# Kernel optimization log

Hardware: AMD Instinct MI355X
Metric: run time of the kernel (lower is better)

The kernel has to match this reference:

```python
import jax, jax.numpy as jnp
import numpy as np

B, S, D = 1, 2048, 2048
H = 16
HD = D // H           # 128
FFN_H = 5632          # int(2*4*D/3) rounded up to multiple of 256
EPS = 1e-5
ROPE_THETA = 10000.0


def rms_norm(x, w, eps=EPS):
    # x * rsqrt(mean(x^2, -1) + eps) * w
    return x * jax.lax.rsqrt(jnp.mean(x * x, axis=-1, keepdims=True) + eps) * w


def apply_rope(x, cos, sin):
    # x: [B, S, H, HD]; cos/sin: [S, HD//2]
    b, s, h, hd = x.shape
    xr = x.reshape(b, s, h, hd // 2, 2)
    x_re, x_im = xr[..., 0], xr[..., 1]
    c = cos[None, :, None, :]
    sn = sin[None, :, None, :]
    o_re = x_re * c - x_im * sn
    o_im = x_re * sn + x_im * c
    return jnp.stack([o_re, o_im], axis=-1).reshape(b, s, h, hd)


def setup_inputs() -> dict:
    key = jax.random.key(0)
    ks = jax.random.split(key, 10)
    x = jax.random.normal(ks[0], (B, S, D), dtype=jnp.float32)
    # RoPE frequencies (Llama-style)
    inv_freq = 1.0 / (ROPE_THETA ** (np.arange(0, HD, 2, dtype=np.float32) / HD))
    angles = np.outer(np.arange(S, dtype=np.float32), inv_freq)  # [S, HD//2]
    freqs_cos = jnp.asarray(np.cos(angles), dtype=jnp.float32)
    freqs_sin = jnp.asarray(np.sin(angles), dtype=jnp.float32)
    # causal mask: 1 = keep, 0 = masked
    mask = jnp.tril(jnp.ones((S, S), dtype=jnp.int32))[None, None]
    sc = 0.02
    return {
        "x": x,
        "freqs_cos": freqs_cos,
        "freqs_sin": freqs_sin,
        "mask": mask,
        "wq": jax.random.normal(ks[1], (D, D), jnp.float32) * sc,
        "wk": jax.random.normal(ks[2], (D, D), jnp.float32) * sc,
        "wv": jax.random.normal(ks[3], (D, D), jnp.float32) * sc,
        "wo": jax.random.normal(ks[4], (D, D), jnp.float32) * sc,
        "w1": jax.random.normal(ks[5], (D, FFN_H), jnp.float32) * sc,
        "w2": jax.random.normal(ks[6], (FFN_H, D), jnp.float32) * sc,
        "w3": jax.random.normal(ks[7], (D, FFN_H), jnp.float32) * sc,
        "attn_norm_w": jnp.ones((D,), jnp.float32),
        "ffn_norm_w": jnp.ones((D,), jnp.float32),
    }


def reference(x, freqs_cos, freqs_sin, mask, wq, wk, wv, wo, w1, w2, w3,
              attn_norm_w, ffn_norm_w):
    b, s, d = x.shape
    # --- attention block ---
    xn = rms_norm(x, attn_norm_w)
    q = (xn @ wq).reshape(b, s, H, HD)
    k = (xn @ wk).reshape(b, s, H, HD)
    v = (xn @ wv).reshape(b, s, H, HD)
    q = apply_rope(q, freqs_cos, freqs_sin)
    k = apply_rope(k, freqs_cos, freqs_sin)
    scores = jnp.einsum('bqhd,bkhd->bhqk', q, k) / jnp.sqrt(jnp.float32(HD))
    scores = jnp.where(mask == 0, -jnp.inf, scores)
    probs = jax.nn.softmax(scores, axis=-1)
    attn = jnp.einsum('bhqk,bkhd->bqhd', probs, v).reshape(b, s, d)
    h = x + attn @ wo
    # --- SwiGLU FFN block ---
    hn = rms_norm(h, ffn_norm_w)
    ff = (jax.nn.silu(hn @ w1) * (hn @ w3)) @ w2
    return h + ff
```

## Files before the change

kernel.cpp:

```cpp
#include <hip/hip_runtime.h>
#include <hip/hip_bf16.h>

typedef __bf16 bf16x8 __attribute__((ext_vector_type(8)));
typedef float f32x4 __attribute__((ext_vector_type(4)));
typedef unsigned short u16x8 __attribute__((ext_vector_type(8)));
typedef unsigned short u16x4 __attribute__((ext_vector_type(4)));

#define DEV static __device__ __forceinline__

DEV unsigned short f2bf(float f) {
    unsigned u = __builtin_bit_cast(unsigned, f);
    u += 0x7fffu + ((u >> 16) & 1u);
    return (unsigned short)(u >> 16);
}
DEV float bf2f(unsigned short h) {
    unsigned u = ((unsigned)h) << 16;
    return __builtin_bit_cast(float, u);
}

DEV void gl2lds16(const void* g, void* l) {
    __builtin_amdgcn_global_load_lds(
        (const __attribute__((address_space(1))) void*)g,
        (__attribute__((address_space(3))) void*)l, 16, 0, 0);
}

#define WAITV(N) asm volatile("s_waitcnt vmcnt(" #N ")" ::: "memory")
#define SBAR()   asm volatile("s_barrier" ::: "memory")

#define STAGE128D(KT, BUF)                                                    \
    _Pragma("unroll")                                                         \
    for (int sl = 0; sl < 3; ++sl) {                                          \
        const unsigned short* sbase = (sl == 0)                               \
            ? A  + (size_t)bm * K                                             \
            : BT + (size_t)(bn + (sl - 1) * 128) * K;                         \
        _Pragma("unroll")                                                     \
        for (int j = 0; j < 2; ++j) {                                         \
            const unsigned short* g = sbase + (size_t)(srow + j * 64) * K     \
                                      + koff + (KT) * 64 + lc;                \
            gl2lds16(g, &lds[BUF][sl][wave * 512 + j * 4096]);                \
        }                                                                     \
    }

#define DSREAD_K(BUF, KK, AR, BR)                                             \
    {                                                                         \
        const char* Ab = (const char*)&lds[BUF][0][0];                        \
        const char* Bb = (const char*)&lds[BUF][1 + (wn >> 1)][0];            \
        _Pragma("unroll")                                                     \
        for (int m4 = 0; m4 < 4; ++m4)                                        \
            AR[m4] = *(const bf16x8*)(Ab +                                    \
                (wm * 64 + m4 * 16 + lr) * 128 +                              \
                (((KK) * 64 + lg * 16) ^ xsw));                               \
        _Pragma("unroll")                                                     \
        for (int n2 = 0; n2 < 4; ++n2)                                        \
            BR[n2] = *(const bf16x8*)(Bb +                                    \
                ((wn & 1) * 64 + n2 * 16 + lr) * 128 +                        \
                (((KK) * 64 + lg * 16) ^ xsw));                               \
    }

#define MFMA16(AR, BR)                                                        \
    __builtin_amdgcn_s_setprio(1);                                            \
    _Pragma("unroll")                                                         \
    for (int m4 = 0; m4 < 4; ++m4)                                            \
        _Pragma("unroll")                                                     \
        for (int n2 = 0; n2 < 4; ++n2)                                        \
            acc[m4][n2] = __builtin_amdgcn_mfma_f32_16x16x32_bf16(            \
                AR[m4], BR[n2], acc[m4][n2], 0, 0, 0);                        \
    __builtin_amdgcn_s_setprio(0);

template <int EPI>
__global__ __launch_bounds__(512, 2)
void gemm128d(const unsigned short* __restrict__ A,
              const unsigned short* __restrict__ BT,
              unsigned short* __restrict__ outB,
              float* __restrict__ outP,
              int M, int N, int K,
              const float* __restrict__ cs, const float* __restrict__ sn,
              unsigned short* __restrict__ vT)
{
    __shared__ alignas(16) unsigned short lds[3][3][8192];
    const int tid  = threadIdx.x;
    const int lane = tid & 63;
    const int wave = tid >> 6;
    const int wm = wave >> 2;
    const int wn = wave & 3;
    const int lr = lane & 15;
    const int lg = lane >> 4;
    const int gy  = gridDim.y;
    const int lin = blockIdx.y * gridDim.x + blockIdx.x;
    const int cpx = (gridDim.x * gy) >> 3;
    const int swz = (lin & 7) * cpx + (lin >> 3);
    const int bm = (swz % gy) * 128;
    const int bn = (swz / gy) * 256;
    const int xsw  = (lr & 7) << 4;
    const int srow = tid >> 3;
    const int lc   = ((tid & 7) ^ (srow & 7)) * 8;
    int koff, NT;
    if constexpr (EPI == 1 || EPI == 3) {
        const int Kh = K >> 1; koff = blockIdx.z * Kh; NT = Kh >> 6;
    } else {
        koff = 0; NT = K >> 6;
    }

    f32x4 acc[4][4] = {};
    bf16x8 a0[4], b0[4], a1[4], b1[4];

    STAGE128D(0, 0);
    STAGE128D(1, 1);
    WAITV(6); SBAR();
    DSREAD_K(0, 0, a0, b0);

    int bc = 0;
    for (int kt = 0; kt < NT - 2; ++kt) {
        const int nb = (bc == 0) ? 2 : bc - 1;
        STAGE128D(kt + 2, nb);
        MFMA16(a0, b0);
        DSREAD_K(bc, 1, a1, b1);
        MFMA16(a1, b1);
        WAITV(6); SBAR();
        const int rb = (bc == 2) ? 0 : bc + 1;
        DSREAD_K(rb, 0, a0, b0);
        bc = rb;
    }
    MFMA16(a0, b0);
    DSREAD_K(bc, 1, a1, b1);
    MFMA16(a1, b1);
    WAITV(0); SBAR();
    {
        const int rb = (bc == 2) ? 0 : bc + 1;
        DSREAD_K(rb, 0, a0, b0);
        bc = rb;
    }
    MFMA16(a0, b0);
    DSREAD_K(bc, 1, a1, b1);
    MFMA16(a1, b1);

#pragma unroll
    for (int m4 = 0; m4 < 4; ++m4) {
        const int row = bm + wm * 64 + m4 * 16 + lg * 4;
#pragma unroll
        for (int n2 = 0; n2 < 4; ++n2) {
            const int col = bn + wn * 64 + n2 * 16 + lr;
            if constexpr (EPI == 4) {
                if (bn >= 4096) {
                    u16x4 o;
#pragma unroll
                    for (int r = 0; r < 4; ++r) o[r] = f2bf(acc[m4][n2][r]);
                    *(u16x4*)(vT + (size_t)(col - 4096) * 2048 + row) = o;
                } else {
#pragma unroll
                    for (int r = 0; r < 4; ++r) {
                        const float v  = acc[m4][n2][r];
                        const float vo = __shfl_xor(v, 1);
                        const int rr = row + r;
                        const int i0 = (col & 127) >> 1;
                        const float c = cs[rr * 64 + i0];
                        const float s = sn[rr * 64 + i0];
                        const float o = (lr & 1) ? (vo * s + v * c)
                                                 : (v * c - vo * s);
                        outB[(size_t)rr * N + col] = f2bf(o);
                    }
                }
            } else {
#pragma unroll
                for (int r = 0; r < 4; ++r) {
                    if constexpr (EPI == 0) {
                        outB[(size_t)(row + r) * N + col] = f2bf(acc[m4][n2][r]);
                    } else if constexpr (EPI == 1) {
                        outP[(size_t)blockIdx.z * M * N + (size_t)(row + r) * N + col] = acc[m4][n2][r];
                    } else if constexpr (EPI == 3) {
                        unsafeAtomicAdd(&outP[(size_t)(row + r) * N + col], acc[m4][n2][r]);
                    } else {
                        const float v  = acc[m4][n2][r];
                        const float vo = __shfl_xor(v, 1);
                        const float x1 = (lr & 1) ? vo : v;
                        const float x3 = (lr & 1) ? v : vo;
                        const float g  = x1 / (1.0f + __expf(-x1)) * x3;
                        if (!(lr & 1))
                            outB[(size_t)(row + r) * (N >> 1) + (col >> 1)] = f2bf(g);
                    }
                }
            }
        }
    }
}

__global__ __launch_bounds__(256)
void reduce2_norm(const float* __restrict__ res, const float* __restrict__ p,
                  const float* __restrict__ w, float* __restrict__ hout,
                  unsigned short* __restrict__ nout)
{
    const int row = blockIdx.x, tid = threadIdx.x;
    const float4* r4 = (const float4*)(res + (size_t)row * 2048);
    const float4* a4 = (const float4*)(p   + (size_t)row * 2048);
    const float4* b4 = (const float4*)(p + (size_t)2048 * 2048 + (size_t)row * 2048);
    float4* h4 = (float4*)(hout + (size_t)row * 2048);
    float4 h[2];
    float ss = 0.f;
#pragma unroll
    for (int i = 0; i < 2; ++i) {
        const int idx = i * 256 + tid;
        const float4 r = r4[idx], a = a4[idx], b = b4[idx];
        float4 v = make_float4(r.x + a.x + b.x, r.y + a.y + b.y,
                               r.z + a.z + b.z, r.w + a.w + b.w);
        h[i] = v; h4[idx] = v;
        ss += v.x * v.x + v.y * v.y + v.z * v.z + v.w * v.w;
    }
#pragma unroll
    for (int off = 32; off; off >>= 1) ss += __shfl_xor(ss, off);
    __shared__ float red[4];
    if ((tid & 63) == 0) red[tid >> 6] = ss;
    __syncthreads();
    const float tot = red[0] + red[1] + red[2] + red[3];
    const float sc = rsqrtf(tot * (1.0f / 2048.0f) + 1e-5f);
#pragma unroll
    for (int i = 0; i < 2; ++i) {
        const int idx = i * 256 + tid;
        const float4 wv = ((const float4*)w)[idx];
        u16x4 o;
        o[0] = f2bf(h[i].x * sc * wv.x); o[1] = f2bf(h[i].y * sc * wv.y);
        o[2] = f2bf(h[i].z * sc * wv.z); o[3] = f2bf(h[i].w * sc * wv.w);
        *(u16x4*)(nout + (size_t)row * 2048 + idx * 4) = o;
    }
}

__global__ __launch_bounds__(256)
void rmsnorm_kernel(const float* __restrict__ x, const float* __restrict__ w,
                    unsigned short* __restrict__ out)
{
    const int row = blockIdx.x;
    const int tid = threadIdx.x;
    const float* xr = x + (size_t)row * 2048;
    const float4 a = *reinterpret_cast<const float4*>(xr + tid * 8);
    const float4 b = *reinterpret_cast<const float4*>(xr + tid * 8 + 4);
    float ss = a.x * a.x + a.y * a.y + a.z * a.z + a.w * a.w
             + b.x * b.x + b.y * b.y + b.z * b.z + b.w * b.w;
#pragma unroll
    for (int off = 32; off; off >>= 1) ss += __shfl_xor(ss, off);
    __shared__ float red[4];
    if ((tid & 63) == 0) red[tid >> 6] = ss;
    __syncthreads();
    const float tot = red[0] + red[1] + red[2] + red[3];
    const float sc = rsqrtf(tot * (1.0f / 2048.0f) + 1e-5f);
    const float4 wa = *reinterpret_cast<const float4*>(w + tid * 8);
    const float4 wb = *reinterpret_cast<const float4*>(w + tid * 8 + 4);
    u16x8 o;
    o[0] = f2bf(a.x * sc * wa.x); o[1] = f2bf(a.y * sc * wa.y);
    o[2] = f2bf(a.z * sc * wa.z); o[3] = f2bf(a.w * sc * wa.w);
    o[4] = f2bf(b.x * sc * wb.x); o[5] = f2bf(b.y * sc * wb.y);
    o[6] = f2bf(b.z * sc * wb.z); o[7] = f2bf(b.w * sc * wb.w);
    *reinterpret_cast<u16x8*>(out + (size_t)row * 2048 + tid * 8) = o;
}

DEV void convT_body(const float* __restrict__ w, unsigned short* __restrict__ wT,
                    int K, int N, int rmul, int radd, int bk, int bn, int tid)
{
    __shared__ unsigned short t[64][66];
    const int r = tid >> 4, c4 = (tid & 15) * 4;
#pragma unroll
    for (int i = 0; i < 4; ++i) {
        const int row = r + i * 16;
        const float4 v = *reinterpret_cast<const float4*>(w + (size_t)(bk + row) * N + bn + c4);
        t[row][c4 + 0] = f2bf(v.x); t[row][c4 + 1] = f2bf(v.y);
        t[row][c4 + 2] = f2bf(v.z); t[row][c4 + 3] = f2bf(v.w);
    }
    __syncthreads();
#pragma unroll
    for (int i = 0; i < 4; ++i) {
        const int n = r + i * 16;
        u16x4 o;
#pragma unroll
        for (int e = 0; e < 4; ++e) o[e] = t[c4 + e][n];
        *reinterpret_cast<u16x4*>(wT + (size_t)(rmul * (bn + n) + radd) * K + bk + c4) = o;
    }
}

__global__ __launch_bounds__(256)
void convT_kernel(const float* __restrict__ w, unsigned short* __restrict__ wT,
                  int K, int N)
{
    convT_body(w, wT, K, N, 1, 0, blockIdx.y * 64, blockIdx.x * 64, threadIdx.x);
}

__global__ __launch_bounds__(256)
void convT4_kernel(const float* __restrict__ w0, const float* __restrict__ w1,
                   const float* __restrict__ w2, const float* __restrict__ w3,
                   unsigned short* __restrict__ wT)
{
    const int z = blockIdx.z;
    const float* w = (z == 0) ? w0 : (z == 1) ? w1 : (z == 2) ? w2 : w3;
    convT_body(w, wT + (size_t)z * 2048 * 2048, 2048, 2048, 1, 0,
               blockIdx.y * 64, blockIdx.x * 64, threadIdx.x);
}

__global__ __launch_bounds__(256)
void convTpair_kernel(const float* __restrict__ wa, const float* __restrict__ wb,
                      unsigned short* __restrict__ wT)
{
    const int z = blockIdx.z;
    convT_body(z ? wb : wa, wT, 2048, 5632, 2, z,
               blockIdx.y * 64, blockIdx.x * 64, threadIdx.x);
}

__global__ __launch_bounds__(512)
void flash_attn(const unsigned short* __restrict__ q,
                const unsigned short* __restrict__ k,
                const unsigned short* __restrict__ vT,
                unsigned short* __restrict__ attn)
{
    __shared__ alignas(16) unsigned short Ks[2][64][136];
    __shared__ alignas(16) unsigned short Vs[2][128][72];
    __shared__ alignas(16) unsigned short Ps[8][16][72];

    const int hh = blockIdx.y;
    const int pi = blockIdx.x;
    const int tid = threadIdx.x;
    const int lane = tid & 63, wave = tid >> 6;
    const int qt = (wave >> 2) ? (31 - pi) : pi;
    const int lr = lane & 15, lg = lane >> 4;
    const int q0 = qt * 64 + (wave & 3) * 16;
    const int myNT = qt + 1;
    const int NT   = 32 - pi;

    const int kr0 = tid >> 4, kc0 = (tid & 15) * 8;
    const int vr0 = tid >> 3, vc0 = (tid & 7) * 8;

    bf16x8 qf[4];
#pragma unroll
    for (int c = 0; c < 4; ++c)
        qf[c] = *reinterpret_cast<const bf16x8*>(
            q + (size_t)(q0 + lr) * 6144 + hh * 128 + c * 32 + lg * 8);

    f32x4 oacc[8] = {};
    float m_r[4], l_r[4];
#pragma unroll
    for (int r = 0; r < 4; ++r) { m_r[r] = -INFINITY; l_r[r] = 0.0f; }
    const float scale = 0.08838834764831845f;

    u16x8 kreg0, kreg1, vreg0, vreg1;
    auto gload = [&](int kt) {
        const int kv0 = kt * 64;
        kreg0 = *reinterpret_cast<const u16x8*>(k + (size_t)(kv0 + kr0) * 6144 + hh * 128 + kc0);
        kreg1 = *reinterpret_cast<const u16x8*>(k + (size_t)(kv0 + kr0 + 32) * 6144 + hh * 128 + kc0);
        vreg0 = *reinterpret_cast<const u16x8*>(vT + (size_t)(hh * 128 + vr0) * 2048 + kv0 + vc0);
        vreg1 = *reinterpret_cast<const u16x8*>(vT + (size_t)(hh * 128 + vr0 + 64) * 2048 + kv0 + vc0);
    };
    auto lwrite = [&](int buf) {
        *reinterpret_cast<u16x8*>(&Ks[buf][kr0][kc0])      = kreg0;
        *reinterpret_cast<u16x8*>(&Ks[buf][kr0 + 32][kc0]) = kreg1;
        *reinterpret_cast<u16x8*>(&Vs[buf][vr0][vc0])      = vreg0;
        *reinterpret_cast<u16x8*>(&Vs[buf][vr0 + 64][vc0]) = vreg1;
    };

    gload(0); lwrite(0);
    __syncthreads();

    for (int kt = 0; kt < NT; ++kt) {
        const int buf = kt & 1;
        if (kt + 1 < NT) gload(kt + 1);

        if (kt < myNT) {
            const int kv0 = kt * 64;
            const bool masked = (kt == myNT - 1);
            f32x4 s[4] = {};
            __builtin_amdgcn_s_setprio(1);
#pragma unroll
            for (int ct = 0; ct < 4; ++ct)
#pragma unroll
                for (int c = 0; c < 4; ++c) {
                    const bf16x8 kf = *reinterpret_cast<const bf16x8*>(
                        &Ks[buf][ct * 16 + lr][c * 32 + lg * 8]);
                    s[ct] = __builtin_amdgcn_mfma_f32_16x16x32_bf16(qf[c], kf, s[ct], 0, 0, 0);
                }
            __builtin_amdgcn_s_setprio(0);
#pragma unroll
            for (int ct = 0; ct < 4; ++ct)
#pragma unroll
                for (int r = 0; r < 4; ++r) {
                    float v = s[ct][r] * scale;
                    if (masked) {
                        const int kvg = kv0 + ct * 16 + lr;
                        const int qg  = q0 + lg * 4 + r;
                        if (kvg > qg) v = -INFINITY;
                    }
                    s[ct][r] = v;
                }
            float mn[4], alpha[4], rs[4];
#pragma unroll
            for (int r = 0; r < 4; ++r) {
                float v = fmaxf(fmaxf(s[0][r], s[1][r]), fmaxf(s[2][r], s[3][r]));
                v = fmaxf(v, __shfl_xor(v, 1));
                v = fmaxf(v, __shfl_xor(v, 2));
                v = fmaxf(v, __shfl_xor(v, 4));
                v = fmaxf(v, __shfl_xor(v, 8));
                mn[r] = fmaxf(m_r[r], v);
                alpha[r] = __expf(m_r[r] - mn[r]);
                m_r[r] = mn[r];
                rs[r] = 0.0f;
            }
#pragma unroll
            for (int ct = 0; ct < 4; ++ct)
#pragma unroll
                for (int r = 0; r < 4; ++r) {
                    const float p = __expf(s[ct][r] - mn[r]);
                    s[ct][r] = p;
                    rs[r] += p;
                }
#pragma unroll
            for (int r = 0; r < 4; ++r) {
                float t2 = rs[r];
                t2 += __shfl_xor(t2, 1);
                t2 += __shfl_xor(t2, 2);
                t2 += __shfl_xor(t2, 4);
                t2 += __shfl_xor(t2, 8);
                l_r[r] = l_r[r] * alpha[r] + t2;
            }
#pragma unroll
            for (int ot = 0; ot < 8; ++ot)
#pragma unroll
                for (int r = 0; r < 4; ++r) oacc[ot][r] *= alpha[r];

#pragma unroll
            for (int ct = 0; ct < 4; ++ct)
#pragma unroll
                for (int r = 0; r < 4; ++r)
                    Ps[wave][lg * 4 + r][ct * 16 + lr] = f2bf(s[ct][r]);

            __builtin_amdgcn_s_setprio(1);
#pragma unroll
            for (int c2 = 0; c2 < 2; ++c2) {
                const bf16x8 pf = *reinterpret_cast<const bf16x8*>(
                    &Ps[wave][lr][c2 * 32 + lg * 8]);
#pragma unroll
                for (int ot = 0; ot < 8; ++ot) {
                    const bf16x8 vf = *reinterpret_cast<const bf16x8*>(
                        &Vs[buf][ot * 16 + lr][c2 * 32 + lg * 8]);
                    oacc[ot] = __builtin_amdgcn_mfma_f32_16x16x32_bf16(pf, vf, oacc[ot], 0, 0, 0);
                }
            }
            __builtin_amdgcn_s_setprio(0);
        }

        if (kt + 1 < NT) lwrite(buf ^ 1);
        __syncthreads();
    }

#pragma unroll
    for (int ot = 0; ot < 8; ++ot)
#pragma unroll
        for (int r = 0; r < 4; ++r) {
            const float v = oacc[ot][r] / l_r[r];
            attn[(size_t)(q0 + lg * 4 + r) * 2048 + hh * 128 + ot * 16 + lr] = f2bf(v);
        }
}

extern "C" void kernel_launch(void* const* d_in, const int* in_sizes, int n_in,
                              void* d_out, int out_size, void* d_ws, size_t ws_size,
                              hipStream_t stream)
{
    const float* x    = (const float*)d_in[0];
    const float* fcos = (const float*)d_in[1];
    const float* fsin = (const float*)d_in[2];
    const float* wq  = (const float*)d_in[4];
    const float* wk  = (const float*)d_in[5];
    const float* wv  = (const float*)d_in[6];
    const float* wo  = (const float*)d_in[7];
    const float* w1  = (const float*)d_in[8];
    const float* w2  = (const float*)d_in[9];
    const float* w3  = (const float*)d_in[10];
    const float* anw = (const float*)d_in[11];
    const float* fnw = (const float*)d_in[12];
    float* out = (float*)d_out;

    char* ws = (char*)d_ws;
    size_t off = 0;
    auto alloc = [&](size_t bytes) { void* p = ws + off; off += bytes; return p; };
    const size_t SZ_DD = (size_t)2048 * 2048 * 2;
    const size_t SZ_DF = (size_t)2048 * 5632 * 2;

    unsigned short* qkvoT = (unsigned short*)alloc(4 * SZ_DD);
    unsigned short* w13T  = (unsigned short*)alloc(2 * SZ_DF);
    unsigned short* w2T   = (unsigned short*)alloc(SZ_DF);

    char* reg1 = (char*)alloc((size_t)48 * 1024 * 1024);
    unsigned short* xn   = (unsigned short*)reg1;
    unsigned short* qkv  = (unsigned short*)(reg1 + SZ_DD);
    unsigned short* vTb  = (unsigned short*)(reg1 + SZ_DD + 3 * SZ_DD);
    unsigned short* ab   = (unsigned short*)(reg1 + SZ_DD + 4 * SZ_DD);
    float*          pk   = (float*)reg1;
    unsigned short* hn   = (unsigned short*)(reg1 + 4 * SZ_DD);

    char* reg2 = (char*)alloc(SZ_DF);
    unsigned short* t1 = (unsigned short*)reg2;

    convT4_kernel<<<dim3(32, 32, 4), 256, 0, stream>>>(wq, wk, wv, wo, qkvoT);
    convTpair_kernel<<<dim3(88, 32, 2), 256, 0, stream>>>(w1, w3, w13T);
    convT_kernel<<<dim3(32, 88), 256, 0, stream>>>(w2, w2T, 5632, 2048);

    rmsnorm_kernel<<<2048, 256, 0, stream>>>(x, anw, xn);
    gemm128d<4><<<dim3(24, 16), 512, 0, stream>>>(xn, qkvoT, qkv, nullptr,
                                                  2048, 6144, 2048, fcos, fsin, vTb);
    flash_attn<<<dim3(16, 16), 512, 0, stream>>>(qkv, qkv + 2048, vTb, ab);
    gemm128d<1><<<dim3(8, 16, 2), 512, 0, stream>>>(ab, qkvoT + 3 * (size_t)2048 * 2048,
                                                    nullptr, pk, 2048, 2048, 2048,
                                                    nullptr, nullptr, nullptr);
    reduce2_norm<<<2048, 256, 0, stream>>>(x, pk, fnw, out, hn);

    gemm128d<2><<<dim3(44, 16), 512, 0, stream>>>(hn, w13T, t1, nullptr,
                                                  2048, 11264, 2048,
                                                  nullptr, nullptr, nullptr);
    gemm128d<3><<<dim3(8, 16, 2), 512, 0, stream>>>(t1, w2T, nullptr, out,
                                                    2048, 2048, 5632,
                                                    nullptr, nullptr, nullptr);
}
```

Measured before the change: 438.0 us.

## Halve GEMM K-tile to 32 to shrink LDS and double occupancy

```diff
diff --git a/kernel.cpp b/kernel.cpp
--- a/kernel.cpp
+++ b/kernel.cpp
@@ -27,34 +27,33 @@
 #define WAITV(N) asm volatile("s_waitcnt vmcnt(" #N ")" ::: "memory")
 #define SBAR()   asm volatile("s_barrier" ::: "memory")
 
-#define STAGE128D(KT, BUF)                                                    \
+#define STAGE32(KT, BUF)                                                      \
     _Pragma("unroll")                                                         \
     for (int sl = 0; sl < 3; ++sl) {                                          \
         const unsigned short* sbase = (sl == 0)                               \
             ? A  + (size_t)bm * K                                             \
             : BT + (size_t)(bn + (sl - 1) * 128) * K;                         \
-        _Pragma("unroll")                                                     \
-        for (int j = 0; j < 2; ++j) {                                         \
-            const unsigned short* g = sbase + (size_t)(srow + j * 64) * K     \
-                                      + koff + (KT) * 64 + lc;                \
-            gl2lds16(g, &lds[BUF][sl][wave * 512 + j * 4096]);                \
-        }                                                                     \
-    }
-
-#define DSREAD_K(BUF, KK, AR, BR)                                             \
+        const unsigned short* g = sbase + (size_t)srow * K                    \
+                                  + koff + (KT) * 32 + lc;                    \
+        gl2lds16(g, &lds[BUF][sl][wave * 512]);                               \
+    }
+
+#define DSREAD32(BUF, AR, BR)                                                 \
     {                                                                         \
         const char* Ab = (const char*)&lds[BUF][0][0];                        \
         const char* Bb = (const char*)&lds[BUF][1 + (wn >> 1)][0];            \
         _Pragma("unroll")                                                     \
-        for (int m4 = 0; m4 < 4; ++m4)                                        \
-            AR[m4] = *(const bf16x8*)(Ab +                                    \
-                (wm * 64 + m4 * 16 + lr) * 128 +                              \
-                (((KK) * 64 + lg * 16) ^ xsw));                               \
+        for (int m4 = 0; m4 < 4; ++m4) {                                      \
+            const int rw = wm * 64 + m4 * 16 + lr;                            \
+            AR[m4] = *(const bf16x8*)(Ab + rw * 64 +                          \
+                     ((lg * 16) ^ (((rw >> 1) & 3) << 4)));                   \
+        }                                                                     \
         _Pragma("unroll")                                                     \
-        for (int n2 = 0; n2 < 4; ++n2)                                        \
-            BR[n2] = *(const bf16x8*)(Bb +                                    \
-                ((wn & 1) * 64 + n2 * 16 + lr) * 128 +                        \
-                (((KK) * 64 + lg * 16) ^ xsw));                               \
+        for (int n2 = 0; n2 < 4; ++n2) {                                      \
+            const int rw = (wn & 1) * 64 + n2 * 16 + lr;                      \
+            BR[n2] = *(const bf16x8*)(Bb + rw * 64 +                          \
+                     ((lg * 16) ^ (((rw >> 1) & 3) << 4)));                   \
+        }                                                                     \
     }
 
 #define MFMA16(AR, BR)                                                        \
@@ -68,7 +67,7 @@
     __builtin_amdgcn_s_setprio(0);
 
 template <int EPI>
-__global__ __launch_bounds__(512, 2)
+__global__ __launch_bounds__(512, 4)
 void gemm128d(const unsigned short* __restrict__ A,
               const unsigned short* __restrict__ BT,
               unsigned short* __restrict__ outB,
@@ -77,7 +76,7 @@
               const float* __restrict__ cs, const float* __restrict__ sn,
               unsigned short* __restrict__ vT)
 {
-    __shared__ alignas(16) unsigned short lds[3][3][8192];
+    __shared__ alignas(16) unsigned short lds[3][3][4096];
     const int tid  = threadIdx.x;
     const int lane = tid & 63;
     const int wave = tid >> 6;
@@ -91,48 +90,40 @@
     const int swz = (lin & 7) * cpx + (lin >> 3);
     const int bm = (swz % gy) * 128;
     const int bn = (swz / gy) * 256;
-    const int xsw  = (lr & 7) << 4;
-    const int srow = tid >> 3;
-    const int lc   = ((tid & 7) ^ (srow & 7)) * 8;
+    const int srow = tid >> 2;
+    const int lc   = (((tid & 3) ^ ((srow >> 1) & 3)) << 3);
     int koff, NT;
     if constexpr (EPI == 1 || EPI == 3) {
-        const int Kh = K >> 1; koff = blockIdx.z * Kh; NT = Kh >> 6;
+        const int Kh = K >> 1; koff = blockIdx.z * Kh; NT = Kh >> 5;
     } else {
-        koff = 0; NT = K >> 6;
+        koff = 0; NT = K >> 5;
     }
 
     f32x4 acc[4][4] = {};
-    bf16x8 a0[4], b0[4], a1[4], b1[4];
-
-    STAGE128D(0, 0);
-    STAGE128D(1, 1);
-    WAITV(6); SBAR();
-    DSREAD_K(0, 0, a0, b0);
+    bf16x8 a_[4], b_[4];
+
+    STAGE32(0, 0);
+    STAGE32(1, 1);
+    WAITV(3); SBAR();
+    DSREAD32(0, a_, b_);
 
     int bc = 0;
     for (int kt = 0; kt < NT - 2; ++kt) {
         const int nb = (bc == 0) ? 2 : bc - 1;
-        STAGE128D(kt + 2, nb);
-        MFMA16(a0, b0);
-        DSREAD_K(bc, 1, a1, b1);
-        MFMA16(a1, b1);
-        WAITV(6); SBAR();
+        STAGE32(kt + 2, nb);
+        MFMA16(a_, b_);
+        WAITV(3); SBAR();
         const int rb = (bc == 2) ? 0 : bc + 1;
-        DSREAD_K(rb, 0, a0, b0);
+        DSREAD32(rb, a_, b_);
         bc = rb;
     }
-    MFMA16(a0, b0);
-    DSREAD_K(bc, 1, a1, b1);
-    MFMA16(a1, b1);
+    MFMA16(a_, b_);
     WAITV(0); SBAR();
     {
         const int rb = (bc == 2) ? 0 : bc + 1;
-        DSREAD_K(rb, 0, a0, b0);
-        bc = rb;
-    }
-    MFMA16(a0, b0);
-    DSREAD_K(bc, 1, a1, b1);
-    MFMA16(a1, b1);
+        DSREAD32(rb, a_, b_);
+    }
+    MFMA16(a_, b_);
 
 #pragma unroll
     for (int m4 = 0; m4 < 4; ++m4) {
```

New measurement: 440.6 us. No clear change (+0.6%).
